# Optimization experiments

Hardware: AMD Instinct MI355X
Metric: run time of the kernel (lower is better)

The kernel has to match this reference:

```python
import jax, jax.numpy as jnp
import numpy as np

# Static config (matches init_kwargs)
B, S, D = 1, 2048, 2048
H, KVH, HD = 16, 4, 128
GROUPS = H // KVH
HEAVY_RATIO = 0.1
RECENT_RATIO = 0.1
SCALE = HD ** -0.5


def setup_inputs() -> dict:
    key = jax.random.key(0)
    ks = jax.random.split(key, 8)
    std = 0.02
    return {
        "hidden_states": jax.random.normal(ks[0], (B, S, D), jnp.float32),
        "q_w": jax.random.normal(ks[1], (D, H * HD), jnp.float32) * std,
        "q_b": jax.random.normal(ks[2], (H * HD,), jnp.float32) * std,
        "k_w": jax.random.normal(ks[3], (D, KVH * HD), jnp.float32) * std,
        "k_b": jax.random.normal(ks[4], (KVH * HD,), jnp.float32) * std,
        "v_w": jax.random.normal(ks[5], (D, KVH * HD), jnp.float32) * std,
        "v_b": jax.random.normal(ks[6], (KVH * HD,), jnp.float32) * std,
        "o_w": jax.random.normal(ks[7], (H * HD, D), jnp.float32) * std,
    }


def reference(hidden_states, q_w, q_b, k_w, k_b, v_w, v_b, o_w):
    # QKV projections -> [B, heads, S, HD]
    q = (hidden_states @ q_w + q_b).reshape(B, S, H, HD).transpose(0, 2, 1, 3)
    k = (hidden_states @ k_w + k_b).reshape(B, S, KVH, HD).transpose(0, 2, 1, 3)
    v = (hidden_states @ v_w + v_b).reshape(B, S, KVH, HD).transpose(0, 2, 1, 3)

    # GQA: repeat KV heads to match query heads (repeat_kv)
    k = jnp.repeat(k, GROUPS, axis=1)  # [B, H, S, HD]
    v = jnp.repeat(v, GROUPS, axis=1)

    # Scaled QK^T with additive causal mask (first call: no H2O mask yet)
    scores = jnp.einsum("bhqd,bhkd->bhqk", q, k) * SCALE
    causal = jnp.tril(jnp.ones((S, S), dtype=bool))
    scores = jnp.where(causal[None, None], scores, jnp.finfo(scores.dtype).min)

    # Softmax in fp32, cast back
    probs = jax.nn.softmax(scores.astype(jnp.float32), axis=-1).astype(q.dtype)

    # H2O heavy-hitter scoring: accumulate attn mass per key, per head
    cur_scores = probs.sum(axis=0).sum(axis=1)  # [H, S]

    heavy_budget = int(HEAVY_RATIO * S)
    recent_budget = int(RECENT_RATIO * S)

    # Eviction mask for next step: keep recent window + top-k heavy hitters
    attn_mask = jnp.ones((H, S + 1), dtype=probs.dtype)
    attn_mask = attn_mask.at[:, : S + 1 - recent_budget].set(0.0)
    selected = cur_scores[:, : S - recent_budget]  # scores outside recent window
    _, keep_topk = jax.lax.top_k(selected, heavy_budget)  # [H, heavy_budget]
    attn_mask = attn_mask.at[jnp.arange(H)[:, None], keep_topk].set(1.0)

    # Attention output + output projection
    out = jnp.einsum("bhqk,bhkd->bhqd", probs, v)
    out = out.transpose(0, 2, 1, 3).reshape(B, S, H * HD) @ o_w
    return out, attn_mask
```

## Files before the change

kernel.cpp:

```cpp
#include <hip/hip_runtime.h>
#include <hip/hip_bf16.h>
#include <math.h>

constexpr int S   = 2048;
constexpr int D   = 2048;
constexpr int H   = 16;
constexpr int KVH = 4;
constexpr int HD  = 128;
constexpr int NQ  = H * HD;
constexpr int NKV = KVH * HD;
constexpr int N3  = NQ + 2 * NKV;
constexpr int GROUPS = H / KVH;
constexpr float SCALE = 0.088388347648318447f;
constexpr int HEAVY  = 204;
constexpr int RECENT = 204;
constexpr int SKEEP  = S - RECENT;
constexpr int MASKC  = S + 1;
constexpr int NTILE_H = 528;

typedef short bf16x8 __attribute__((ext_vector_type(8)));
typedef _Float16 f16x8 __attribute__((ext_vector_type(8)));
typedef unsigned short ushort8 __attribute__((ext_vector_type(8)));
typedef unsigned short ushort4v __attribute__((ext_vector_type(4)));
typedef float f32x4 __attribute__((ext_vector_type(4)));

__device__ __forceinline__ unsigned short f2b(float x) {
  __hip_bfloat16 h = __float2bfloat16(x);
  return *(unsigned short*)&h;
}
__device__ __forceinline__ float b2f(unsigned short u) {
  __hip_bfloat16 h = *(__hip_bfloat16*)&u;
  return __bfloat162float(h);
}
__device__ __forceinline__ unsigned short f2h(float x) {
  _Float16 h = (_Float16)x;
  return *(unsigned short*)&h;
}

__device__ __forceinline__ void gload16(const unsigned short* g,
                                        unsigned short* l) {
  __builtin_amdgcn_global_load_lds(
      (const __attribute__((address_space(1))) unsigned int*)g,
      (__attribute__((address_space(3))) unsigned int*)l, 16, 0, 0);
}

__device__ __forceinline__ void split_wT_dev(
    const float* __restrict__ in, unsigned short* __restrict__ oh,
    int K, int N, int rowOff, int ldOut, int bx, int by, float (*Lt)[65]) {
  const int n0 = bx * 64, k0 = by * 64;
  const int t = threadIdx.x;
  const int cq = t & 15, r4 = t >> 4;
#pragma unroll
  for (int i = 0; i < 4; ++i) {
    int r = r4 + i * 16;
    float4 v = *(const float4*)&in[(size_t)(k0 + r) * N + n0 + cq * 4];
    Lt[cq * 4 + 0][r] = v.x;
    Lt[cq * 4 + 1][r] = v.y;
    Lt[cq * 4 + 2][r] = v.z;
    Lt[cq * 4 + 3][r] = v.w;
  }
  __syncthreads();
#pragma unroll
  for (int i = 0; i < 4; ++i) {
    int rr = r4 + i * 16;
    size_t base = (size_t)(rowOff + n0 + rr) * ldOut + k0 + cq * 4;
    ushort4v hv;
#pragma unroll
    for (int j = 0; j < 4; ++j) hv[j] = f2h(Lt[rr][cq * 4 + j]);
    *(ushort4v*)&oh[base] = hv;
  }
}

__global__ __launch_bounds__(256) void prep_all(
    const float* __restrict__ hs, const float* __restrict__ q_w,
    const float* __restrict__ k_w, const float* __restrict__ v_w,
    const float* __restrict__ o_w, const float* __restrict__ qb,
    const float* __restrict__ kb, const float* __restrict__ vb,
    unsigned short* __restrict__ hsh,
    unsigned short* __restrict__ WTh,
    unsigned short* __restrict__ OTh, float* __restrict__ bcat) {
  __shared__ float Lt[64][65];
  const int b = blockIdx.x;
  if (b < 1024) {
    split_wT_dev(q_w, WTh, D, NQ, 0, D, b & 31, b >> 5, Lt);
  } else if (b < 1280) {
    int b2 = b - 1024;
    split_wT_dev(k_w, WTh, D, NKV, NQ, D, b2 & 7, b2 >> 3, Lt);
  } else if (b < 1536) {
    int b2 = b - 1280;
    split_wT_dev(v_w, WTh, D, NKV, NQ + NKV, D, b2 & 7, b2 >> 3, Lt);
  } else if (b < 2560) {
    int b2 = b - 1536;
    const int n0 = (b2 & 31) * 64, k0 = (b2 >> 5) * 64;
    const int t = threadIdx.x;
    const int cq = t & 15, r4 = t >> 4;
#pragma unroll
    for (int i = 0; i < 4; ++i) {
      int r = r4 + i * 16;
      float4 v = *(const float4*)&o_w[(size_t)(k0 + r) * D + n0 + cq * 4];
      Lt[cq * 4 + 0][r] = v.x;
      Lt[cq * 4 + 1][r] = v.y;
      Lt[cq * 4 + 2][r] = v.z;
      Lt[cq * 4 + 3][r] = v.w;
    }
    __syncthreads();
#pragma unroll
    for (int i = 0; i < 4; ++i) {
      int rr = r4 + i * 16;
      size_t base = (size_t)(n0 + rr) * NQ + k0 + cq * 4;
      ushort4v hv;
#pragma unroll
      for (int j = 0; j < 4; ++j) hv[j] = f2b(Lt[rr][cq * 4 + j]);
      *(ushort4v*)&OTh[base] = hv;
    }
  } else if (b < 3072) {
    int b2 = b - 2560;
    size_t base = (size_t)b2 * 8192;
    for (int i = threadIdx.x * 4; i < 8192; i += 1024) {
      float4 v = *(const float4*)&hs[base + i];
      ushort4v hv;
      hv[0] = f2h(v.x);
      hv[1] = f2h(v.y);
      hv[2] = f2h(v.z);
      hv[3] = f2h(v.w);
      *(ushort4v*)&hsh[base + i] = hv;
    }
  } else {
    int i = (b - 3072) * 256 + threadIdx.x;
    if (i < NQ) bcat[i] = qb[i];
    else if (i < NQ + NKV) bcat[i] = kb[i - NQ];
    else if (i < N3) bcat[i] = vb[i - NQ - NKV];
  }
}

__global__ __launch_bounds__(256) void gemm_qkv(
    const unsigned short* __restrict__ Ah,
    const unsigned short* __restrict__ Bh,
    const float* __restrict__ bias,
    unsigned short* __restrict__ Qh,
    unsigned short* __restrict__ Kh,
    unsigned short* __restrict__ Vt, int M, int N, int K) {
  __shared__ __align__(16) unsigned short sA[2][128 * 32];
  __shared__ __align__(16) unsigned short sB[2][96 * 32];
  const int tid = threadIdx.x;
  const int lane = tid & 63, wave = tid >> 6;
  const int wm = wave >> 1, wn = wave & 1;
  const int quad = lane >> 4, l16 = lane & 15;
  const int m0 = blockIdx.y * 128, n0 = blockIdx.x * 96;

  const int lr = lane >> 2;
  const int gj = (lane & 3) ^ (lr & 3);

  f32x4 acc[4][3];
#pragma unroll
  for (int i = 0; i < 4; ++i)
#pragma unroll
    for (int j = 0; j < 3; ++j) acc[i][j] = (f32x4){0.f, 0.f, 0.f, 0.f};

#pragma unroll
  for (int it = 0; it < 2; ++it) {
    int c = wave * 2 + it;
    int r = c * 16 + lr;
    size_t ga = (size_t)(m0 + r) * K + gj * 8;
    gload16(&Ah[ga], &sA[0][c * 512]);
  }
#pragma unroll
  for (int it = 0; it < 2; ++it) {
    int c = wave + it * 4;
    if (c < 6) {
      int r = c * 16 + lr;
      size_t gb = (size_t)(n0 + r) * K + gj * 8;
      gload16(&Bh[gb], &sB[0][c * 512]);
    }
  }
  __syncthreads();

  int cur = 0;
  for (int k0 = 0; k0 < K; k0 += 32, cur ^= 1) {
    if (k0 + 32 < K) {
      const int kn = k0 + 32;
#pragma unroll
      for (int it = 0; it < 2; ++it) {
        int c = wave * 2 + it;
        int r = c * 16 + lr;
        size_t ga = (size_t)(m0 + r) * K + kn + gj * 8;
        gload16(&Ah[ga], &sA[cur ^ 1][c * 512]);
      }
#pragma unroll
      for (int it = 0; it < 2; ++it) {
        int c = wave + it * 4;
        if (c < 6) {
          int r = c * 16 + lr;
          size_t gb = (size_t)(n0 + r) * K + kn + gj * 8;
          gload16(&Bh[gb], &sB[cur ^ 1][c * 512]);
        }
      }
    }
    const int sw = (quad ^ (l16 & 3)) * 8;
    f16x8 fa[4], fb[3];
#pragma unroll
    for (int i = 0; i < 4; ++i)
      fa[i] = *(f16x8*)&sA[cur][(wm * 64 + i * 16 + l16) * 32 + sw];
#pragma unroll
    for (int j = 0; j < 3; ++j)
      fb[j] = *(f16x8*)&sB[cur][(wn * 48 + j * 16 + l16) * 32 + sw];
#pragma unroll
    for (int i = 0; i < 4; ++i)
#pragma unroll
      for (int j = 0; j < 3; ++j)
        acc[i][j] = __builtin_amdgcn_mfma_f32_16x16x32_f16(fa[i], fb[j], acc[i][j], 0, 0, 0);
    __syncthreads();
  }
#pragma unroll
  for (int i = 0; i < 4; ++i) {
#pragma unroll
    for (int j = 0; j < 3; ++j) {
      int row = m0 + wm * 64 + i * 16 + quad * 4;
      int col = n0 + wn * 48 + j * 16 + l16;
      float bv = bias[col];
      if (col < NQ) {
#pragma unroll
        for (int r = 0; r < 4; ++r) {
          size_t o = (size_t)(row + r) * NQ + col;
          Qh[o] = f2h(acc[i][j][r] + bv);
        }
      } else if (col < NQ + NKV) {
        int c = col - NQ;
        size_t ob = ((size_t)(c >> 7) * S) * HD + (c & 127);
#pragma unroll
        for (int r = 0; r < 4; ++r) {
          size_t o = ob + (size_t)(row + r) * HD;
          Kh[o] = f2h(acc[i][j][r] + bv);
        }
      } else {
        int c = col - NQ - NKV;
        ushort4v pv;
#pragma unroll
        for (int r = 0; r < 4; ++r) pv[r] = f2h(acc[i][j][r] + bv);
        *(ushort4v*)&Vt[((size_t)(c >> 7) * HD + (c & 127)) * S + row] = pv;
      }
    }
  }
}

__global__ __launch_bounds__(256) void fuse_post(
    const unsigned short* __restrict__ AOh, const unsigned short* __restrict__ OTh,
    float* __restrict__ C,
    const unsigned short* __restrict__ Eg, const float* __restrict__ lbuf,
    float* __restrict__ cur) {
  __shared__ __align__(16) unsigned char smem[32768];
  const int bid = blockIdx.x;
  const int tid = threadIdx.x;
  if (bid < 256) {
    unsigned short* sAb = (unsigned short*)smem;
    unsigned short* sBb = (unsigned short*)smem + 8192;
    const int lane = tid & 63, wave = tid >> 6;
    const int wm = wave >> 1, wn = wave & 1;
    const int quad = lane >> 4, l16 = lane & 15;
    const int m0 = (bid >> 4) * 128, n0 = (bid & 15) * 128;
    const int K = NQ, N = D;
    const int lr = lane >> 2;
    const int gj = (lane & 3) ^ (lr & 3);

    f32x4 acc[4][4];
#pragma unroll
    for (int i = 0; i < 4; ++i)
#pragma unroll
      for (int j = 0; j < 4; ++j) acc[i][j] = (f32x4){0.f, 0.f, 0.f, 0.f};

#pragma unroll
    for (int it = 0; it < 2; ++it) {
      int c = wave * 2 + it;
      int r = c * 16 + lr;
      size_t ga = (size_t)(m0 + r) * K + gj * 8;
      size_t gb = (size_t)(n0 + r) * K + gj * 8;
      gload16(&AOh[ga], &sAb[c * 512]);
      gload16(&OTh[gb], &sBb[c * 512]);
    }
    __syncthreads();

    int cb = 0;
    for (int k0 = 0; k0 < K; k0 += 32, cb ^= 1) {
      if (k0 + 32 < K) {
        const int kn = k0 + 32;
#pragma unroll
        for (int it = 0; it < 2; ++it) {
          int c = wave * 2 + it;
          int r = c * 16 + lr;
          size_t ga = (size_t)(m0 + r) * K + kn + gj * 8;
          size_t gb = (size_t)(n0 + r) * K + kn + gj * 8;
          gload16(&AOh[ga], &sAb[(cb ^ 1) * 4096 + c * 512]);
          gload16(&OTh[gb], &sBb[(cb ^ 1) * 4096 + c * 512]);
        }
      }
      const int sw = (quad ^ (l16 & 3)) * 8;
      bf16x8 fa[4], fb[4];
#pragma unroll
      for (int i = 0; i < 4; ++i) {
        fa[i] = *(bf16x8*)&sAb[cb * 4096 + (wm * 64 + i * 16 + l16) * 32 + sw];
        fb[i] = *(bf16x8*)&sBb[cb * 4096 + (wn * 64 + i * 16 + l16) * 32 + sw];
      }
#pragma unroll
      for (int i = 0; i < 4; ++i)
#pragma unroll
        for (int j = 0; j < 4; ++j)
          acc[i][j] = __builtin_amdgcn_mfma_f32_16x16x32_bf16(fa[i], fb[j], acc[i][j], 0, 0, 0);
      __syncthreads();
    }
#pragma unroll
    for (int i = 0; i < 4; ++i)
#pragma unroll
      for (int j = 0; j < 4; ++j) {
        int row = m0 + wm * 64 + i * 16 + quad * 4;
        int col = n0 + wn * 64 + j * 16 + l16;
#pragma unroll
        for (int r = 0; r < 4; ++r)
          C[(size_t)(row + r) * N + col] = acc[i][j][r];
      }
  } else {
    const int bid2 = bid - 256;
    const int kt = bid2 % 29;
    const int h  = bid2 / 29;
    const int c8 = tid & 7, qg = tid >> 3;
    float acc[8];
#pragma unroll
    for (int j = 0; j < 8; ++j) acc[j] = 0.f;
    const size_t hb = (size_t)h * NTILE_H;
    for (int qt = kt; qt < 32; ++qt) {
      size_t tb = (hb + (size_t)(qt * (qt + 1) / 2) + kt) * 4096;
      float li0 = 1.0f / lbuf[h * S + qt * 64 + qg];
      float li1 = 1.0f / lbuf[h * S + qt * 64 + 32 + qg];
      f16x8 e0 = *(const f16x8*)&Eg[tb + (size_t)qg * 64 + c8 * 8];
      f16x8 e1 = *(const f16x8*)&Eg[tb + (size_t)(32 + qg) * 64 + c8 * 8];
#pragma unroll
      for (int j = 0; j < 8; ++j)
        acc[j] += (float)e0[j] * li0 + (float)e1[j] * li1;
    }
    float (*red)[8] = (float(*)[8])smem;
#pragma unroll
    for (int j = 0; j < 8; ++j) red[tid][j] = acc[j];
    __syncthreads();
    if (tid < 64) {
      int cc = tid >> 3, j = tid & 7;
      float s = 0.f;
#pragma unroll
      for (int g = 0; g < 32; ++g) s += red[cc + 8 * g][j];
      cur[h * S + kt * 64 + cc * 8 + j] = s;
    }
  }
}

__global__ __launch_bounds__(256) void gemm_bf16(
    const unsigned short* __restrict__ Ah, const unsigned short* __restrict__ Bh,
    float* __restrict__ C, int M, int N, int K) {
  __shared__ __align__(16) unsigned short sA[2][128 * 32];
  __shared__ __align__(16) unsigned short sB[2][128 * 32];
  const int tid = threadIdx.x;
  const int lane = tid & 63, wave = tid >> 6;
  const int wm = wave >> 1, wn = wave & 1;
  const int quad = lane >> 4, l16 = lane & 15;
  const int m0 = blockIdx.y * 128, n0 = blockIdx.x * 128;
  const int lr = lane >> 2;
  const int gj = (lane & 3) ^ (lr & 3);

  f32x4 acc[4][4];
#pragma unroll
  for (int i = 0; i < 4; ++i)
#pragma unroll
    for (int j = 0; j < 4; ++j) acc[i][j] = (f32x4){0.f, 0.f, 0.f, 0.f};

#pragma unroll
  for (int it = 0; it < 2; ++it) {
    int c = wave * 2 + it;
    int r = c * 16 + lr;
    size_t ga = (size_t)(m0 + r) * K + gj * 8;
    size_t gb = (size_t)(n0 + r) * K + gj * 8;
    gload16(&Ah[ga], &sA[0][c * 512]);
    gload16(&Bh[gb], &sB[0][c * 512]);
  }
  __syncthreads();

  int cur = 0;
  for (int k0 = 0; k0 < K; k0 += 32, cur ^= 1) {
    if (k0 + 32 < K) {
      const int kn = k0 + 32;
#pragma unroll
      for (int it = 0; it < 2; ++it) {
        int c = wave * 2 + it;
        int r = c * 16 + lr;
        size_t ga = (size_t)(m0 + r) * K + kn + gj * 8;
        size_t gb = (size_t)(n0 + r) * K + kn + gj * 8;
        gload16(&Ah[ga], &sA[cur ^ 1][c * 512]);
        gload16(&Bh[gb], &sB[cur ^ 1][c * 512]);
      }
    }
    const int sw = (quad ^ (l16 & 3)) * 8;
    bf16x8 fa[4], fb[4];
#pragma unroll
    for (int i = 0; i < 4; ++i) {
      fa[i] = *(bf16x8*)&sA[cur][(wm * 64 + i * 16 + l16) * 32 + sw];
      fb[i] = *(bf16x8*)&sB[cur][(wn * 64 + i * 16 + l16) * 32 + sw];
    }
#pragma unroll
    for (int i = 0; i < 4; ++i)
#pragma unroll
      for (int j = 0; j < 4; ++j)
        acc[i][j] = __builtin_amdgcn_mfma_f32_16x16x32_bf16(fa[i], fb[j], acc[i][j], 0, 0, 0);
    __syncthreads();
  }
#pragma unroll
  for (int i = 0; i < 4; ++i)
#pragma unroll
    for (int j = 0; j < 4; ++j) {
      int row = m0 + wm * 64 + i * 16 + quad * 4;
      int col = n0 + wn * 64 + j * 16 + l16;
#pragma unroll
      for (int r = 0; r < 4; ++r)
        C[(size_t)(row + r) * N + col] = acc[i][j][r];
    }
}

__global__ __launch_bounds__(256) void attn_mfma(
    const unsigned short* __restrict__ Qh,
    const unsigned short* __restrict__ Kh,
    const unsigned short* __restrict__ Vt, unsigned short* __restrict__ AOh,
    float* __restrict__ lbuf, unsigned short* __restrict__ Eg) {
  const int x = blockIdx.x;
  const int base = x & 255;
  const int qt0 = base & 31, h0 = base >> 5;
  const int qt = (x < 256) ? qt0 : 31 - qt0;
  const int h  = (x < 256) ? h0 : h0 + 8;
  const int kvh = h / GROUPS;
  const int tid = threadIdx.x;
  const int lane = tid & 63, w = tid >> 6;
  const int quad = lane >> 4, l16 = lane & 15;
  const int q0 = qt * 64;

  __shared__ __align__(16) unsigned short smem[22528];
  unsigned short* sQ  = smem;
  unsigned short* sK  = smem;
  unsigned short* sVt = smem + 8704;
  unsigned short* sP  = smem + 17920;

  const size_t ebase = ((size_t)h * NTILE_H + (size_t)(qt * (qt + 1) / 2)) * 4096;

  ushort8 pK[4], pV[4];
#pragma unroll
  for (int it = 0; it < 4; ++it) {
    int idx = tid + it * 256;
    int r = idx >> 4, c8 = idx & 15;
    size_t g = ((size_t)kvh * S + r) * HD + c8 * 8;
    pK[it] = *(const ushort8*)&Kh[g];
  }
#pragma unroll
  for (int it = 0; it < 4; ++it) {
    int idx = tid + it * 256;
    int d = idx >> 3, c8 = idx & 7;
    size_t g = ((size_t)kvh * HD + d) * S + c8 * 8;
    pV[it] = *(const ushort8*)&Vt[g];
  }

#pragma unroll
  for (int it = 0; it < 4; ++it) {
    int idx = tid + it * 256;
    int r = idx >> 4, c8 = idx & 15;
    size_t g = (size_t)(q0 + r) * NQ + h * HD + c8 * 8;
    *(ushort8*)&sQ[r * 136 + c8 * 8] = *(const ushort8*)&Qh[g];
  }
  __syncthreads();
  f16x8 fq[4];
#pragma unroll
  for (int d4 = 0; d4 < 4; ++d4)
    fq[d4] = *(f16x8*)&sQ[(w * 16 + l16) * 136 + d4 * 32 + quad * 8];

  f32x4 O[8];
#pragma unroll
  for (int jn = 0; jn < 8; ++jn) O[jn] = (f32x4){0.f, 0.f, 0.f, 0.f};
  float l_[4] = {0.f, 0.f, 0.f, 0.f};

  const int row_l = w * 16 + quad * 4;
  const int wbase = w * 1152;

  for (int kt = 0; kt <= qt; ++kt) {
    __syncthreads();
#pragma unroll
    for (int it = 0; it < 4; ++it) {
      int idx = tid + it * 256;
      int r = idx >> 4, c8 = idx & 15;
      *(ushort8*)&sK[r * 136 + c8 * 8] = pK[it];
    }
#pragma unroll
    for (int it = 0; it < 4; ++it) {
      int idx = tid + it * 256;
      int d = idx >> 3, c8 = idx & 7;
      *(ushort8*)&sVt[d * 72 + c8 * 8] = pV[it];
    }
    __syncthreads();
    if (kt < qt) {
#pragma unroll
      for (int it = 0; it < 4; ++it) {
        int idx = tid + it * 256;
        int r = idx >> 4, c8 = idx & 15;
        size_t g = ((size_t)kvh * S + (kt + 1) * 64 + r) * HD + c8 * 8;
        pK[it] = *(const ushort8*)&Kh[g];
      }
#pragma unroll
      for (int it = 0; it < 4; ++it) {
        int idx = tid + it * 256;
        int d = idx >> 3, c8 = idx & 7;
        size_t g = ((size_t)kvh * HD + d) * S + (kt + 1) * 64 + c8 * 8;
        pV[it] = *(const ushort8*)&Vt[g];
      }
    }

    f32x4 sc[4];
#pragma unroll
    for (int j = 0; j < 4; ++j) sc[j] = (f32x4){0.f, 0.f, 0.f, 0.f};
#pragma unroll
    for (int d4 = 0; d4 < 4; ++d4) {
#pragma unroll
      for (int j = 0; j < 4; ++j) {
        f16x8 bk = *(f16x8*)&sK[(j * 16 + l16) * 136 + d4 * 32 + quad * 8];
        sc[j] = __builtin_amdgcn_mfma_f32_16x16x32_f16(fq[d4], bk, sc[j], 0, 0, 0);
      }
    }
    const bool diag = (kt == qt);
#pragma unroll
    for (int j = 0; j < 4; ++j) {
      int col_l = j * 16 + l16;
#pragma unroll
      for (int r = 0; r < 4; ++r) {
        float v = sc[j][r] * SCALE;
        if (diag && col_l > row_l + r) v = -INFINITY;
        float p = __expf(v);
        sc[j][r] = p;
        l_[r] += p;
      }
    }
#pragma unroll
    for (int j = 0; j < 4; ++j)
#pragma unroll
      for (int r = 0; r < 4; ++r)
        sP[wbase + (quad * 4 + r) * 72 + j * 16 + l16] = f2h(sc[j][r]);

    if (Eg) {
      size_t tb = ebase + (size_t)kt * 4096;
#pragma unroll
      for (int it2 = 0; it2 < 2; ++it2) {
        int ci = lane + it2 * 64;
        int row = ci >> 3, cc = ci & 7;
        *(ushort8*)&Eg[tb + (size_t)(w * 16 + row) * 64 + cc * 8] =
            *(ushort8*)&sP[wbase + row * 72 + cc * 8];
      }
    }

    f16x8 ap0 = *(f16x8*)&sP[wbase + l16 * 72 + quad * 8];
    f16x8 ap1 = *(f16x8*)&sP[wbase + l16 * 72 + 32 + quad * 8];
#pragma unroll
    for (int jn = 0; jn < 8; ++jn) {
      f16x8 bv0 = *(f16x8*)&sVt[(jn * 16 + l16) * 72 + quad * 8];
      f16x8 bv1 = *(f16x8*)&sVt[(jn * 16 + l16) * 72 + 32 + quad * 8];
      O[jn] = __builtin_amdgcn_mfma_f32_16x16x32_f16(ap0, bv0, O[jn], 0, 0, 0);
      O[jn] = __builtin_amdgcn_mfma_f32_16x16x32_f16(ap1, bv1, O[jn], 0, 0, 0);
    }
  }
#pragma unroll
  for (int off = 1; off < 16; off <<= 1)
#pragma unroll
    for (int r = 0; r < 4; ++r) l_[r] += __shfl_xor(l_[r], off);
  float linv[4];
#pragma unroll
  for (int r = 0; r < 4; ++r) linv[r] = 1.0f / l_[r];
#pragma unroll
  for (int jn = 0; jn < 8; ++jn)
#pragma unroll
    for (int r = 0; r < 4; ++r)
      AOh[(size_t)(q0 + row_l + r) * NQ + h * HD + jn * 16 + l16] =
          f2b(O[jn][r] * linv[r]);
  if (l16 == 0) {
#pragma unroll
    for (int r = 0; r < 4; ++r)
      lbuf[h * S + q0 + row_l + r] = l_[r];
  }
}

__global__ __launch_bounds__(256) void cur_mfma(
    const unsigned short* __restrict__ Qh,
    const unsigned short* __restrict__ Kh,
    const float* __restrict__ lbuf, float* __restrict__ cur) {
  const int x = blockIdx.x;
  const int base = x & 255;
  const int kt0 = base & 31, h0 = base >> 5;
  const int kt = (x < 256) ? kt0 : 31 - kt0;
  const int h  = (x < 256) ? h0 : h0 + 8;
  const int kvh = h / GROUPS;
  const int tid = threadIdx.x;
  const int lane = tid & 63, w = tid >> 6;
  const int quad = lane >> 4, l16 = lane & 15;

  __shared__ __align__(16) unsigned short sKh[8704];
  __shared__ __align__(16) unsigned short sQh[8704];
  __shared__ float slinv[64];

#pragma unroll
  for (int it = 0; it < 4; ++it) {
    int idx = tid + it * 256;
    int r = idx >> 4, c8 = idx & 15;
    size_t g = ((size_t)kvh * S + kt * 64 + r) * HD + c8 * 8;
    *(ushort8*)&sKh[r * 136 + c8 * 8] = *(const ushort8*)&Kh[g];
  }
  __syncthreads();
  f16x8 fk[4];
#pragma unroll
  for (int d4 = 0; d4 < 4; ++d4)
    fk[d4] = *(f16x8*)&sKh[(w * 16 + l16) * 136 + d4 * 32 + quad * 8];

  const int krow_l = w * 16 + quad * 4;
  float csum[4] = {0.f, 0.f, 0.f, 0.f};

  ushort8 pQ[4];
  float pli = 0.f;
#pragma unroll
  for (int it = 0; it < 4; ++it) {
    int idx = tid + it * 256;
    int r = idx >> 4, c8 = idx & 15;
    size_t g = (size_t)(kt * 64 + r) * NQ + h * HD + c8 * 8;
    pQ[it] = *(const ushort8*)&Qh[g];
  }
  if (tid < 64) pli = 1.0f / lbuf[h * S + kt * 64 + tid];

  for (int qt = kt; qt < S / 64; ++qt) {
    __syncthreads();
#pragma unroll
    for (int it = 0; it < 4; ++it) {
      int idx = tid + it * 256;
      int r = idx >> 4, c8 = idx & 15;
      *(ushort8*)&sQh[r * 136 + c8 * 8] = pQ[it];
    }
    if (tid < 64) slinv[tid] = pli;
    __syncthreads();
    if (qt + 1 < S / 64) {
#pragma unroll
      for (int it = 0; it < 4; ++it) {
        int idx = tid + it * 256;
        int r = idx >> 4, c8 = idx & 15;
        size_t g = (size_t)((qt + 1) * 64 + r) * NQ + h * HD + c8 * 8;
        pQ[it] = *(const ushort8*)&Qh[g];
      }
      if (tid < 64) pli = 1.0f / lbuf[h * S + (qt + 1) * 64 + tid];
    }
    f32x4 sc[4];
#pragma unroll
    for (int j = 0; j < 4; ++j) sc[j] = (f32x4){0.f, 0.f, 0.f, 0.f};
#pragma unroll
    for (int d4 = 0; d4 < 4; ++d4) {
#pragma unroll
      for (int j = 0; j < 4; ++j) {
        f16x8 bq = *(f16x8*)&sQh[(j * 16 + l16) * 136 + d4 * 32 + quad * 8];
        sc[j] = __builtin_amdgcn_mfma_f32_16x16x32_f16(fk[d4], bq, sc[j], 0, 0, 0);
      }
    }
    const bool diag = (qt == kt);
#pragma unroll
    for (int j = 0; j < 4; ++j) {
      int qcol_l = j * 16 + l16;
      float lv = slinv[qcol_l];
#pragma unroll
      for (int r = 0; r < 4; ++r) {
        float p = __expf(sc[j][r] * SCALE) * lv;
        if (diag && (krow_l + r) > qcol_l) p = 0.f;
        csum[r] += p;
      }
    }
  }
#pragma unroll
  for (int off = 1; off < 16; off <<= 1)
#pragma unroll
    for (int r = 0; r < 4; ++r) csum[r] += __shfl_xor(csum[r], off);
  if (l16 == 0) {
#pragma unroll
    for (int r = 0; r < 4; ++r)
      cur[h * S + kt * 64 + krow_l + r] = csum[r];
  }
}

__global__ __launch_bounds__(256) void topk_kernel(
    const float* __restrict__ cur, float* __restrict__ mask) {
  const int h = blockIdx.x;
  const int tid = threadIdx.x;
  const int lane = tid & 63, w = tid >> 6;
  __shared__ unsigned uv[SKEEP];
  __shared__ int redw[4];
  __shared__ int wsum[4];

  for (int i = tid; i < SKEEP; i += 256) uv[i] = __float_as_uint(cur[h * S + i]);
  __syncthreads();

  unsigned lo = 0u, hi = 0xffffffffu;
  while (lo < hi) {
    unsigned mid = (unsigned)((((unsigned long long)lo + hi) + 1ull) >> 1);
    int c = 0;
    for (int i = tid; i < SKEEP; i += 256) c += (uv[i] >= mid) ? 1 : 0;
#pragma unroll
    for (int off = 1; off < 64; off <<= 1) c += __shfl_xor(c, off);
    if (lane == 0) redw[w] = c;
    __syncthreads();
    int cnt = redw[0] + redw[1] + redw[2] + redw[3];
    __syncthreads();
    if (cnt >= HEAVY) lo = mid; else hi = mid - 1;
  }
  const unsigned vk = lo;
  int c = 0;
  for (int i = tid; i < SKEEP; i += 256) c += (uv[i] > vk) ? 1 : 0;
#pragma unroll
  for (int off = 1; off < 64; off <<= 1) c += __shfl_xor(c, off);
  if (lane == 0) redw[w] = c;
  __syncthreads();
  const int cgt = redw[0] + redw[1] + redw[2] + redw[3];
  const int rem = HEAVY - cgt;

  for (int j = tid; j < MASKC; j += 256)
    mask[(size_t)h * MASKC + j] = (j >= MASKC - RECENT) ? 1.0f : 0.0f;
  __syncthreads();
  for (int i = tid; i < SKEEP; i += 256)
    if (uv[i] > vk) mask[(size_t)h * MASKC + i] = 1.0f;

  constexpr int PER = (SKEEP + 255) / 256;
  int i0 = tid * PER;
  int i1 = i0 + PER;
  if (i0 > SKEEP) i0 = SKEEP;
  if (i1 > SKEEP) i1 = SKEEP;
  int myT = 0;
  for (int i = i0; i < i1; ++i) myT += (uv[i] == vk) ? 1 : 0;
  int v = myT;
#pragma unroll
  for (int off = 1; off < 64; off <<= 1) {
    int t = __shfl_up(v, off);
    if (lane >= off) v += t;
  }
  if (lane == 63) wsum[w] = v;
  __syncthreads();
  int wOff = 0;
  for (int k = 0; k < w; ++k) wOff += wsum[k];
  int excl = wOff + v - myT;
  for (int i = i0; i < i1; ++i) {
    if (uv[i] == vk) {
      if (excl < rem) mask[(size_t)h * MASKC + i] = 1.0f;
      ++excl;
    }
  }
}

extern "C" void kernel_launch(void* const* d_in, const int* in_sizes, int n_in,
                              void* d_out, int out_size, void* d_ws,
                              size_t ws_size, hipStream_t stream) {
  const float* hs  = (const float*)d_in[0];
  const float* q_w = (const float*)d_in[1];
  const float* q_b = (const float*)d_in[2];
  const float* k_w = (const float*)d_in[3];
  const float* k_b = (const float*)d_in[4];
  const float* v_w = (const float*)d_in[5];
  const float* v_b = (const float*)d_in[6];
  const float* o_w = (const float*)d_in[7];

  char* ws = (char*)d_ws;
  unsigned short* Qh   = (unsigned short*)(ws + 0);
  unsigned short* Kh   = (unsigned short*)(ws + 16777216);
  unsigned short* Vt   = (unsigned short*)(ws + 20971520);
  unsigned short* AOh  = (unsigned short*)(ws + 25165824);
  float* lb   = (float*)(ws + 33685504);
  float* cur  = (float*)(ws + 33816576);
  float* bcat = (float*)(ws + 33947648);
  char* pool = ws + 33959936;
  unsigned short* hsh = (unsigned short*)pool;
  unsigned short* WTh = (unsigned short*)(pool + 16777216);
  unsigned short* OTh = (unsigned short*)(pool + 41943040);

  const size_t E_OFF = 84291584ull;
  const size_t E_SZ  = (size_t)H * NTILE_H * 4096 * 2;
  const bool use_e = (ws_size >= E_OFF + E_SZ);
  unsigned short* Eg = use_e ? (unsigned short*)(ws + E_OFF) : nullptr;

  float* outp  = (float*)d_out;
  float* maskp = outp + (size_t)S * D;

  dim3 blk(256);
  prep_all<<<dim3(3084), blk, 0, stream>>>(hs, q_w, k_w, v_w, o_w, q_b, k_b,
                                           v_b, hsh, WTh, OTh, bcat);
  gemm_qkv<<<dim3(N3 / 96, S / 128), blk, 0, stream>>>(
      hsh, WTh, bcat, Qh, Kh, Vt, S, N3, D);
  attn_mfma<<<dim3(512), blk, 0, stream>>>(Qh, Kh, Vt, AOh, lb, Eg);
  if (use_e) {
    fuse_post<<<dim3(256 + 29 * 16), blk, 0, stream>>>(AOh, OTh, outp, Eg, lb,
                                                       cur);
    topk_kernel<<<dim3(H), blk, 0, stream>>>(cur, maskp);
  } else {
    cur_mfma<<<dim3(512), blk, 0, stream>>>(Qh, Kh, lb, cur);
    topk_kernel<<<dim3(H), blk, 0, stream>>>(cur, maskp);
    gemm_bf16<<<dim3(D / 128, S / 128), blk, 0, stream>>>(AOh, OTh, outp, S, D,
                                                          NQ);
  }
}
```

Baseline: 249.6 us.

## Read K/V MFMA operands directly from global memory instead of LDS staging

The attention kernel no longer stages Q, K and V^T tiles through shared memory with register prefetch and two barriers per iteration. Each wave instead loads its MFMA B-operands straight from global memory (relying on L1/L2 cache for reuse across the 4 waves), and shared memory shrinks to just the P buffer. This removes the LDS writes and the per-tile __syncthreads, and may raise occupancy. The cost is that each wave re-reads the same K/V data from global memory, without explicit prefetch to hide latency.

```diff
diff --git a/kernel.cpp b/kernel.cpp
--- a/kernel.cpp
+++ b/kernel.cpp
@@ -436,42 +436,17 @@
   const int quad = lane >> 4, l16 = lane & 15;
   const int q0 = qt * 64;
 
-  __shared__ __align__(16) unsigned short smem[22528];
-  unsigned short* sQ  = smem;
-  unsigned short* sK  = smem;
-  unsigned short* sVt = smem + 8704;
-  unsigned short* sP  = smem + 17920;
+  __shared__ __align__(16) unsigned short sP[4608];
 
   const size_t ebase = ((size_t)h * NTILE_H + (size_t)(qt * (qt + 1) / 2)) * 4096;
-
-  ushort8 pK[4], pV[4];
-#pragma unroll
-  for (int it = 0; it < 4; ++it) {
-    int idx = tid + it * 256;
-    int r = idx >> 4, c8 = idx & 15;
-    size_t g = ((size_t)kvh * S + r) * HD + c8 * 8;
-    pK[it] = *(const ushort8*)&Kh[g];
-  }
-#pragma unroll
-  for (int it = 0; it < 4; ++it) {
-    int idx = tid + it * 256;
-    int d = idx >> 3, c8 = idx & 7;
-    size_t g = ((size_t)kvh * HD + d) * S + c8 * 8;
-    pV[it] = *(const ushort8*)&Vt[g];
-  }
-
-#pragma unroll
-  for (int it = 0; it < 4; ++it) {
-    int idx = tid + it * 256;
-    int r = idx >> 4, c8 = idx & 15;
-    size_t g = (size_t)(q0 + r) * NQ + h * HD + c8 * 8;
-    *(ushort8*)&sQ[r * 136 + c8 * 8] = *(const ushort8*)&Qh[g];
-  }
-  __syncthreads();
+  const unsigned short* Kb = Kh + (size_t)kvh * S * HD;
+  const unsigned short* Vb = Vt + (size_t)kvh * HD * S;
+
   f16x8 fq[4];
 #pragma unroll
   for (int d4 = 0; d4 < 4; ++d4)
-    fq[d4] = *(f16x8*)&sQ[(w * 16 + l16) * 136 + d4 * 32 + quad * 8];
+    fq[d4] = *(const f16x8*)&Qh[(size_t)(q0 + w * 16 + l16) * NQ + h * HD +
+                                d4 * 32 + quad * 8];
 
   f32x4 O[8];
 #pragma unroll
@@ -482,37 +457,6 @@
   const int wbase = w * 1152;
 
   for (int kt = 0; kt <= qt; ++kt) {
-    __syncthreads();
-#pragma unroll
-    for (int it = 0; it < 4; ++it) {
-      int idx = tid + it * 256;
-      int r = idx >> 4, c8 = idx & 15;
-      *(ushort8*)&sK[r * 136 + c8 * 8] = pK[it];
-    }
-#pragma unroll
-    for (int it = 0; it < 4; ++it) {
-      int idx = tid + it * 256;
-      int d = idx >> 3, c8 = idx & 7;
-      *(ushort8*)&sVt[d * 72 + c8 * 8] = pV[it];
-    }
-    __syncthreads();
-    if (kt < qt) {
-#pragma unroll
-      for (int it = 0; it < 4; ++it) {
-        int idx = tid + it * 256;
-        int r = idx >> 4, c8 = idx & 15;
-        size_t g = ((size_t)kvh * S + (kt + 1) * 64 + r) * HD + c8 * 8;
-        pK[it] = *(const ushort8*)&Kh[g];
-      }
-#pragma unroll
-      for (int it = 0; it < 4; ++it) {
-        int idx = tid + it * 256;
-        int d = idx >> 3, c8 = idx & 7;
-        size_t g = ((size_t)kvh * HD + d) * S + (kt + 1) * 64 + c8 * 8;
-        pV[it] = *(const ushort8*)&Vt[g];
-      }
-    }
-
     f32x4 sc[4];
 #pragma unroll
     for (int j = 0; j < 4; ++j) sc[j] = (f32x4){0.f, 0.f, 0.f, 0.f};
@@ -520,7 +464,8 @@
     for (int d4 = 0; d4 < 4; ++d4) {
 #pragma unroll
       for (int j = 0; j < 4; ++j) {
-        f16x8 bk = *(f16x8*)&sK[(j * 16 + l16) * 136 + d4 * 32 + quad * 8];
+        f16x8 bk = *(const f16x8*)&Kb[(size_t)(kt * 64 + j * 16 + l16) * HD +
+                                      d4 * 32 + quad * 8];
         sc[j] = __builtin_amdgcn_mfma_f32_16x16x32_f16(fq[d4], bk, sc[j], 0, 0, 0);
       }
     }
@@ -558,8 +503,10 @@
     f16x8 ap1 = *(f16x8*)&sP[wbase + l16 * 72 + 32 + quad * 8];
 #pragma unroll
     for (int jn = 0; jn < 8; ++jn) {
-      f16x8 bv0 = *(f16x8*)&sVt[(jn * 16 + l16) * 72 + quad * 8];
-      f16x8 bv1 = *(f16x8*)&sVt[(jn * 16 + l16) * 72 + 32 + quad * 8];
+      f16x8 bv0 = *(const f16x8*)&Vb[(size_t)(jn * 16 + l16) * S + kt * 64 +
+                                     quad * 8];
+      f16x8 bv1 = *(const f16x8*)&Vb[(size_t)(jn * 16 + l16) * S + kt * 64 +
+                                     32 + quad * 8];
       O[jn] = __builtin_amdgcn_mfma_f32_16x16x32_f16(ap0, bv0, O[jn], 0, 0, 0);
       O[jn] = __builtin_amdgcn_mfma_f32_16x16x32_f16(ap1, bv1, O[jn], 0, 0, 0);
     }
```

Result: slower. 402.2 us (+61.2%).
